# Optimization experiments

Measured on AMD Instinct MI355X. Metric: run time of the kernel, lower is better.

## Reference

```python
import jax, jax.numpy as jnp
import numpy as np

NEG_BIG = -9e15
ALPHA = 0.2  # leakyrelu negative slope

N, F_IN, F_OUT = 8192, 512, 64


def setup_inputs() -> dict:
    key = jax.random.key(0)
    k1, k2, k3, k4 = jax.random.split(key, 4)
    input = jax.random.normal(k1, (N, F_IN), dtype=jnp.float32)
    adj = jax.random.randint(k2, (N, N), 0, 2, dtype=jnp.int32)
    W = jax.random.normal(k3, (F_IN, F_OUT), dtype=jnp.float32) * 0.05
    a = jax.random.normal(k4, (2 * F_OUT, 1), dtype=jnp.float32) * 0.1
    return {"input": input, "adj": adj, "W": W, "a": a}


def reference(input, adj, W, a):
    # h: [N, F_out]
    h = input @ W
    # The original builds a_input[i,j] = concat(h_i, h_j) and dots with a.
    # Decompose: e_ij = leakyrelu(h_i @ a_src + h_j @ a_dst) -- identical math,
    # avoids the N*N*2F intermediate.
    a_src = a[:F_OUT, 0]  # [F_out]
    a_dst = a[F_OUT:, 0]  # [F_out]
    s_src = h @ a_src     # [N]
    s_dst = h @ a_dst     # [N]
    e = jax.nn.leaky_relu(s_src[:, None] + s_dst[None, :], negative_slope=ALPHA)  # [N, N]
    masked = jnp.where(adj > 0, e, jnp.float32(NEG_BIG))
    attention = jax.nn.softmax(masked, axis=1)  # dropout omitted (eval mode)
    h_prime = attention @ h  # [N, F_out]
    return jax.nn.elu(h_prime)  # concat=True
```

## Files before the change

kernel.cpp:

```cpp
#include <hip/hip_runtime.h>
#include <hip/hip_bf16.h>

namespace {
constexpr int kN    = 8192;
constexpr int kFin  = 512;
constexpr int kFout = 64;
constexpr float kAlpha = 0.2f;
constexpr int kJSplit = 8;
constexpr int kJLen   = kN / kJSplit;
constexpr int kChunks = kJLen / 32;
constexpr int kTileParts = 2;

using bf16x8 = __attribute__((ext_vector_type(8))) short;
using f32x4  = __attribute__((ext_vector_type(4))) float;

__device__ __forceinline__ unsigned short f2bf(float x) {
  return __builtin_bit_cast(unsigned short, __float2bfloat16(x));
}
__device__ __forceinline__ float lrelu(float x) {
  return fmaxf(x, kAlpha * x);
}
__device__ __forceinline__ unsigned int fkey(float x) {
  unsigned int b = __float_as_uint(x);
  return (b & 0x80000000u) ? ~b : (b | 0x80000000u);
}
__device__ __forceinline__ float fdec(unsigned int k) {
  return (k & 0x80000000u) ? __uint_as_float(k ^ 0x80000000u) : __uint_as_float(~k);
}
}

__global__ __launch_bounds__(256) void k_wt(const float* __restrict__ W,
                                            float* __restrict__ WT,
                                            unsigned int* __restrict__ Smax_u) {
  const int gid = blockIdx.x * 256 + threadIdx.x;
  if (gid == 0) *Smax_u = 0u;
  const int k = gid >> 6, f = gid & 63;
  WT[(size_t)f * kFin + k] = W[gid];
}

__global__ __launch_bounds__(256) void k_linear(
    const float* __restrict__ X, const float* __restrict__ WT, const float* __restrict__ A,
    unsigned short* __restrict__ hTf, float* __restrict__ s_src, float* __restrict__ s_dst,
    unsigned int* __restrict__ Smax_u)
{
  const int t = threadIdx.x;
  const int wv = t >> 6, f = t & 63;
  const int i0 = blockIdx.x * 16;

  __shared__ float Xlds[16 * kFin];
  __shared__ unsigned short h_sm[16][64];
  __shared__ float red[4];

  {
    const float4* Xg = (const float4*)(X + (size_t)i0 * kFin);
    float4* Xl = (float4*)Xlds;
    float4 v0 = Xg[t +   0], v1 = Xg[t + 256], v2 = Xg[t +  512], v3 = Xg[t +  768];
    float4 v4 = Xg[t +1024], v5 = Xg[t +1280], v6 = Xg[t + 1536], v7 = Xg[t + 1792];
    Xl[t +    0] = v0; Xl[t +  256] = v1; Xl[t +  512] = v2; Xl[t +  768] = v3;
    Xl[t + 1024] = v4; Xl[t + 1280] = v5; Xl[t + 1536] = v6; Xl[t + 1792] = v7;
  }
  __syncthreads();

  const int r0l = wv * 4;
  const float* w0 = WT + (size_t)f * kFin;
  float acc0 = 0.f, acc1 = 0.f, acc2 = 0.f, acc3 = 0.f;
  float4 wb0 = *(const float4*)(w0 + 0);
  float4 wb1 = *(const float4*)(w0 + 4);
  const float* xr = Xlds + r0l * kFin;
  for (int k = 0; k < kFin; k += 4) {
    const float4 wc = (k & 4) ? wb1 : wb0;
    if (k + 8 < kFin) {
      const float4 wn = *(const float4*)(w0 + k + 8);
      if (k & 4) wb1 = wn; else wb0 = wn;
    }
    const float4 xa = *(const float4*)(xr + k);
    const float4 xb = *(const float4*)(xr + kFin + k);
    const float4 xc = *(const float4*)(xr + 2 * kFin + k);
    const float4 xd = *(const float4*)(xr + 3 * kFin + k);
#pragma unroll
    for (int j = 0; j < 4; ++j) {
      const float wk = ((const float*)&wc)[j];
      acc0 = fmaf(((const float*)&xa)[j], wk, acc0);
      acc1 = fmaf(((const float*)&xb)[j], wk, acc1);
      acc2 = fmaf(((const float*)&xc)[j], wk, acc2);
      acc3 = fmaf(((const float*)&xd)[j], wk, acc3);
    }
  }

  const float asrc = A[f], adst = A[kFout + f];
  float accs[4] = {acc0, acc1, acc2, acc3};
  float dmax = -3.4e38f;
#pragma unroll
  for (int r = 0; r < 4; ++r) {
    float vs = accs[r] * asrc;
    float vd = accs[r] * adst;
#pragma unroll
    for (int off = 32; off > 0; off >>= 1) {
      vs += __shfl_xor(vs, off, 64);
      vd += __shfl_xor(vd, off, 64);
    }
    if (f == 0) {
      s_src[i0 + r0l + r] = vs;
      s_dst[i0 + r0l + r] = vd;
      dmax = fmaxf(dmax, vd);
    }
    h_sm[r0l + r][f] = f2bf(accs[r]);
  }
  if (f == 0) red[wv] = dmax;
  __syncthreads();
  if (t == 0) {
    float m = fmaxf(fmaxf(red[0], red[1]), fmaxf(red[2], red[3]));
    atomicMax(Smax_u, fkey(m));
  }

  if (t < 128) {
    const int jblk = i0 >> 5, half = (i0 >> 4) & 1;
    const int w = t >> 5, li = t & 31;
    const int lane = half * 32 + li;
    const int ql = li >> 4, fcol = w * 16 + (li & 15);
    bf16x8 v;
#pragma unroll
    for (int e = 0; e < 8; ++e) v[e] = (short)h_sm[ql * 8 + e][fcol];
    *(bf16x8*)(hTf + (size_t)jblk * 2048 + w * 512 + (size_t)lane * 8) = v;
  }
}

__global__ __launch_bounds__(256) void k_attn(
    const int* __restrict__ adj, const unsigned short* __restrict__ hTf,
    const float* __restrict__ s_src, const float* __restrict__ s_dst,
    const unsigned int* __restrict__ Smax_u, float* __restrict__ accp,
    float* __restrict__ lp)
{
  const int t = threadIdx.x;
  const int wv = t >> 6, lane = t & 63;
  const int wid = blockIdx.x * 4 + wv;
  const int tile = wid >> 3;
  const int q    = wid & 7;
  const int i0 = tile * 16, jbase = q * kJLen;
  const int row = lane & 15, quad = lane >> 4;

  __shared__ float sacc[4][16][64];
  __shared__ float sl[4][16];

  const float S = fdec(*Smax_u);
  const float ssrc = s_src[i0 + row];
  const float mr = lrelu(ssrc + S);

  const int4*   aptr = (const int4*)(adj + (size_t)(i0 + row) * kN + jbase + quad * 8);
  const float4* dptr = (const float4*)(s_dst + jbase + quad * 8);
  const unsigned short* hbase = hTf + (size_t)(jbase >> 5) * 2048 + (size_t)lane * 8;

  float l_acc = 0.f;
  f32x4 acc0 = {0.f, 0.f, 0.f, 0.f};
  f32x4 acc1 = {0.f, 0.f, 0.f, 0.f};
  f32x4 acc2 = {0.f, 0.f, 0.f, 0.f};
  f32x4 acc3 = {0.f, 0.f, 0.f, 0.f};

  int4   Aa0 = aptr[0],  Aa1 = aptr[1];
  float4 Da0 = dptr[0],  Da1 = dptr[1];
  int4   Ab0 = aptr[8],  Ab1 = aptr[9];
  float4 Db0 = dptr[8],  Db1 = dptr[9];

  auto body = [&](int c, int4& A0, int4& A1, float4& D0, float4& D1)
      __attribute__((always_inline)) {
    const unsigned short* hp = hbase + (size_t)c * 2048;
    const uint4 hv0 = *(const uint4*)(hp +    0);
    const uint4 hv1 = *(const uint4*)(hp +  512);
    const uint4 hv2 = *(const uint4*)(hp + 1024);
    const uint4 hv3 = *(const uint4*)(hp + 1536);

    float pv[8];
    {
      const int*   aa = (const int*)&A0;
      const float* dd = (const float*)&D0;
#pragma unroll
      for (int j = 0; j < 4; ++j) {
        const float e = lrelu(ssrc + dd[j]);
        pv[j] = aa[j] > 0 ? __expf(e - mr) : 0.f;
      }
      aa = (const int*)&A1; dd = (const float*)&D1;
#pragma unroll
      for (int j = 0; j < 4; ++j) {
        const float e = lrelu(ssrc + dd[j]);
        pv[4 + j] = aa[j] > 0 ? __expf(e - mr) : 0.f;
      }
    }

    {
      const int cn = (c + 2) & (kChunks - 1);
      A0 = aptr[cn * 8];  A1 = aptr[cn * 8 + 1];
      D0 = dptr[cn * 8];  D1 = dptr[cn * 8 + 1];
    }

    l_acc += ((pv[0] + pv[1]) + (pv[2] + pv[3])) +
             ((pv[4] + pv[5]) + (pv[6] + pv[7]));
    bf16x8 pa;
#pragma unroll
    for (int j = 0; j < 8; ++j) pa[j] = (short)f2bf(pv[j]);

    acc0 = __builtin_amdgcn_mfma_f32_16x16x32_bf16(pa, __builtin_bit_cast(bf16x8, hv0), acc0, 0, 0, 0);
    acc1 = __builtin_amdgcn_mfma_f32_16x16x32_bf16(pa, __builtin_bit_cast(bf16x8, hv1), acc1, 0, 0, 0);
    acc2 = __builtin_amdgcn_mfma_f32_16x16x32_bf16(pa, __builtin_bit_cast(bf16x8, hv2), acc2, 0, 0, 0);
    acc3 = __builtin_amdgcn_mfma_f32_16x16x32_bf16(pa, __builtin_bit_cast(bf16x8, hv3), acc3, 0, 0, 0);
  };

  for (int c = 0; c < kChunks; c += 2) {
    body(c,     Aa0, Aa1, Da0, Da1);
    body(c + 1, Ab0, Ab1, Db0, Db1);
  }

  float lv = l_acc;
  lv += __shfl_xor(lv, 16, 64);
  lv += __shfl_xor(lv, 32, 64);
  if (lane < 16) sl[wv][lane] = lv;

  {
    float* ab = &sacc[wv][0][0];
#pragma unroll
    for (int reg = 0; reg < 4; ++reg) {
      ab[(quad * 4 + reg) * 64 +  0 + row] = acc0[reg];
      ab[(quad * 4 + reg) * 64 + 16 + row] = acc1[reg];
      ab[(quad * 4 + reg) * 64 + 32 + row] = acc2[reg];
      ab[(quad * 4 + reg) * 64 + 48 + row] = acc3[reg];
    }
  }
  __syncthreads();

  {
    const float* sb = &sacc[0][0][0];
    float* gout = accp + (size_t)blockIdx.x * 16 * 64;
#pragma unroll
    for (int k = 0; k < 4; ++k) {
      const int idx = t + k * 256;
      gout[idx] = (sb[idx] + sb[1024 + idx]) + (sb[2048 + idx] + sb[3072 + idx]);
    }
    if (t < 16) {
      lp[(size_t)blockIdx.x * 16 + t] =
          (sl[0][t] + sl[1][t]) + (sl[2][t] + sl[3][t]);
    }
  }
}

__global__ __launch_bounds__(256) void k_comb(const float* __restrict__ accp,
                                              const float* __restrict__ lp,
                                              float* __restrict__ out)
{
  const int gid = blockIdx.x * 256 + threadIdx.x;
  const int i = gid >> 6, f = gid & 63;
  const int ib = i >> 4, il = i & 15;
  const int b0 = ib * kTileParts;
  float a = 0.f, l = 0.f;
#pragma unroll
  for (int p = 0; p < kTileParts; ++p) {
    a += accp[((size_t)(b0 + p) * 16 + il) * 64 + f];
    l += lp[(size_t)(b0 + p) * 16 + il];
  }
  float v = a / l;
  v = v > 0.f ? v : __expf(v) - 1.f;
  out[gid] = v;
}

extern "C" void kernel_launch(void* const* d_in, const int* in_sizes, int n_in,
                              void* d_out, int out_size, void* d_ws, size_t ws_size,
                              hipStream_t stream) {
  const float* X   = (const float*)d_in[0];
  const int*   adj = (const int*)d_in[1];
  const float* W   = (const float*)d_in[2];
  const float* A   = (const float*)d_in[3];
  float* out = (float*)d_out;

  char* ws = (char*)d_ws;
  unsigned short* hTf = (unsigned short*)ws;  ws += (size_t)kN * kFout * 2;
  float* WT    = (float*)ws;                  ws += (size_t)kFout * kFin * 4;
  float* s_src = (float*)ws;                  ws += kN * 4;
  float* s_dst = (float*)ws;                  ws += kN * 4;
  unsigned int* Smax_u = (unsigned int*)ws;   ws += 256;
  float* accp  = (float*)ws;                  ws += (size_t)(kN / 16) * kTileParts * 16 * 64 * 4;
  float* lp    = (float*)ws;

  k_wt    <<<kFin * kFout / 256, 256, 0, stream>>>(W, WT, Smax_u);
  k_linear<<<kN / 16, 256, 0, stream>>>(X, WT, A, hTf, s_src, s_dst, Smax_u);
  k_attn  <<<(kN / 16) * kJSplit / 4, 256, 0, stream>>>(adj, hTf, s_src, s_dst, Smax_u, accp, lp);
  k_comb  <<<kN * kFout / 256, 256, 0, stream>>>(accp, lp, out);
}
```

Baseline: 443.2 us.

## Coalesce adj loads by row-contiguous lanes and transpose P through LDS

Lanes now map 8 lanes per adj row, each reading one int4, so a row's 32-element chunk is one contiguous 128-byte access. Previously each lane read two int4 at a 32-byte stride across quads. The bf16 probabilities are written to a per-wave double-buffered LDS tile and read back in MFMA A-operand layout. This adds an LDS round trip per chunk and relies on wave-level ordering without explicit barriers. It also adds s_setprio around the MFMAs and a launch-bounds occupancy hint of 4.

```diff
diff --git a/kernel.cpp b/kernel.cpp
--- a/kernel.cpp
+++ b/kernel.cpp
@@ -11,6 +11,7 @@
 constexpr int kChunks = kJLen / 32;
 constexpr int kTileParts = 2;
 
+using bf16x4 = __attribute__((ext_vector_type(4))) short;
 using bf16x8 = __attribute__((ext_vector_type(8))) short;
 using f32x4  = __attribute__((ext_vector_type(4))) float;
 
@@ -125,7 +126,7 @@
   }
 }
 
-__global__ __launch_bounds__(256) void k_attn(
+__global__ __launch_bounds__(256, 4) void k_attn(
     const int* __restrict__ adj, const unsigned short* __restrict__ hTf,
     const float* __restrict__ s_src, const float* __restrict__ s_dst,
     const unsigned int* __restrict__ Smax_u, float* __restrict__ accp,
@@ -137,31 +138,35 @@
   const int tile = wid >> 3;
   const int q    = wid & 7;
   const int i0 = tile * 16, jbase = q * kJLen;
+  const int lr = lane >> 3;
+  const int lg = lane & 7;
   const int row = lane & 15, quad = lane >> 4;
 
+  __shared__ unsigned short Pl[4][2][16][40];
   __shared__ float sacc[4][16][64];
   __shared__ float sl[4][16];
 
   const float S = fdec(*Smax_u);
-  const float ssrc = s_src[i0 + row];
-  const float mr = lrelu(ssrc + S);
-
-  const int4*   aptr = (const int4*)(adj + (size_t)(i0 + row) * kN + jbase + quad * 8);
-  const float4* dptr = (const float4*)(s_dst + jbase + quad * 8);
+  const float sA = s_src[i0 + lr];
+  const float sB = s_src[i0 + 8 + lr];
+  const float mA = lrelu(sA + S);
+  const float mB = lrelu(sB + S);
+
+  const int4* aA = (const int4*)(adj + (size_t)(i0 + lr) * kN + jbase) + lg;
+  const int4* aB = (const int4*)(adj + (size_t)(i0 + 8 + lr) * kN + jbase) + lg;
+  const float4* dp = (const float4*)(s_dst + jbase) + lg;
   const unsigned short* hbase = hTf + (size_t)(jbase >> 5) * 2048 + (size_t)lane * 8;
 
-  float l_acc = 0.f;
+  float l_accA = 0.f, l_accB = 0.f;
   f32x4 acc0 = {0.f, 0.f, 0.f, 0.f};
   f32x4 acc1 = {0.f, 0.f, 0.f, 0.f};
   f32x4 acc2 = {0.f, 0.f, 0.f, 0.f};
   f32x4 acc3 = {0.f, 0.f, 0.f, 0.f};
 
-  int4   Aa0 = aptr[0],  Aa1 = aptr[1];
-  float4 Da0 = dptr[0],  Da1 = dptr[1];
-  int4   Ab0 = aptr[8],  Ab1 = aptr[9];
-  float4 Db0 = dptr[8],  Db1 = dptr[9];
-
-  auto body = [&](int c, int4& A0, int4& A1, float4& D0, float4& D1)
+  int4   Aa = aA[0], Ba = aB[0];  float4 Da = dp[0];
+  int4   Ab = aA[8], Bb = aB[8];  float4 Db = dp[8];
+
+  auto body = [&](int c, int sbuf, int4& A, int4& B, float4& D)
       __attribute__((always_inline)) {
     const unsigned short* hp = hbase + (size_t)c * 2048;
     const uint4 hv0 = *(const uint4*)(hp +    0);
@@ -169,50 +174,60 @@
     const uint4 hv2 = *(const uint4*)(hp + 1024);
     const uint4 hv3 = *(const uint4*)(hp + 1536);
 
-    float pv[8];
+    float pvA[4], pvB[4];
     {
-      const int*   aa = (const int*)&A0;
-      const float* dd = (const float*)&D0;
+      const int*   ia = (const int*)&A;
+      const int*   ib = (const int*)&B;
+      const float* dd = (const float*)&D;
 #pragma unroll
       for (int j = 0; j < 4; ++j) {
-        const float e = lrelu(ssrc + dd[j]);
-        pv[j] = aa[j] > 0 ? __expf(e - mr) : 0.f;
+        const float eA = lrelu(sA + dd[j]);
+        const float eB = lrelu(sB + dd[j]);
+        pvA[j] = ia[j] > 0 ? __expf(eA - mA) : 0.f;
+        pvB[j] = ib[j] > 0 ? __expf(eB - mB) : 0.f;
       }
-      aa = (const int*)&A1; dd = (const float*)&D1;
-#pragma unroll
-      for (int j = 0; j < 4; ++j) {
-        const float e = lrelu(ssrc + dd[j]);
-        pv[4 + j] = aa[j] > 0 ? __expf(e - mr) : 0.f;
-      }
-    }
+    }
+    l_accA += (pvA[0] + pvA[1]) + (pvA[2] + pvA[3]);
+    l_accB += (pvB[0] + pvB[1]) + (pvB[2] + pvB[3]);
+
+    bf16x4 wA, wB;
+#pragma unroll
+    for (int j = 0; j < 4; ++j) {
+      wA[j] = (short)f2bf(pvA[j]);
+      wB[j] = (short)f2bf(pvB[j]);
+    }
+    *(bf16x4*)&Pl[wv][sbuf][lr][lg * 4]     = wA;
+    *(bf16x4*)&Pl[wv][sbuf][8 + lr][lg * 4] = wB;
 
     {
       const int cn = (c + 2) & (kChunks - 1);
-      A0 = aptr[cn * 8];  A1 = aptr[cn * 8 + 1];
-      D0 = dptr[cn * 8];  D1 = dptr[cn * 8 + 1];
-    }
-
-    l_acc += ((pv[0] + pv[1]) + (pv[2] + pv[3])) +
-             ((pv[4] + pv[5]) + (pv[6] + pv[7]));
-    bf16x8 pa;
-#pragma unroll
-    for (int j = 0; j < 8; ++j) pa[j] = (short)f2bf(pv[j]);
-
+      A = aA[cn * 8];  B = aB[cn * 8];  D = dp[cn * 8];
+    }
+
+    const bf16x8 pa = *(const bf16x8*)&Pl[wv][sbuf][row][quad * 8];
+    __builtin_amdgcn_s_setprio(1);
     acc0 = __builtin_amdgcn_mfma_f32_16x16x32_bf16(pa, __builtin_bit_cast(bf16x8, hv0), acc0, 0, 0, 0);
     acc1 = __builtin_amdgcn_mfma_f32_16x16x32_bf16(pa, __builtin_bit_cast(bf16x8, hv1), acc1, 0, 0, 0);
     acc2 = __builtin_amdgcn_mfma_f32_16x16x32_bf16(pa, __builtin_bit_cast(bf16x8, hv2), acc2, 0, 0, 0);
     acc3 = __builtin_amdgcn_mfma_f32_16x16x32_bf16(pa, __builtin_bit_cast(bf16x8, hv3), acc3, 0, 0, 0);
+    __builtin_amdgcn_s_setprio(0);
   };
 
   for (int c = 0; c < kChunks; c += 2) {
-    body(c,     Aa0, Aa1, Da0, Da1);
-    body(c + 1, Ab0, Ab1, Db0, Db1);
-  }
-
-  float lv = l_acc;
-  lv += __shfl_xor(lv, 16, 64);
-  lv += __shfl_xor(lv, 32, 64);
-  if (lane < 16) sl[wv][lane] = lv;
+    body(c,     0, Aa, Ba, Da);
+    body(c + 1, 1, Ab, Bb, Db);
+  }
+
+  l_accA += __shfl_xor(l_accA, 1, 64);
+  l_accA += __shfl_xor(l_accA, 2, 64);
+  l_accA += __shfl_xor(l_accA, 4, 64);
+  l_accB += __shfl_xor(l_accB, 1, 64);
+  l_accB += __shfl_xor(l_accB, 2, 64);
+  l_accB += __shfl_xor(l_accB, 4, 64);
+  if (lg == 0) {
+    sl[wv][lr]     = l_accA;
+    sl[wv][8 + lr] = l_accB;
+  }
 
   {
     float* ab = &sacc[wv][0][0];
```

Measured after the change: 430.7 us. 2.8% less time.
